# Performance work log

Measured on AMD Instinct MI355X. Metric: run time of the kernel, lower is better.

Reference implementation:

```python
import jax, jax.numpy as jnp
import numpy as np

N, P1, P2, D = 4, 8192, 8192, 3
BIG = 1e10  # masks out padded target points before top-k (pytorch3d uses +inf)


def setup_inputs() -> dict:
    key = jax.random.key(0)
    k1, k2, k3 = jax.random.split(key, 3)
    pred_points = jax.random.normal(k1, (N, P1, D), dtype=jnp.float32)
    target_points = jax.random.normal(k2, (N, P2, D), dtype=jnp.float32)
    # ragged target lengths in [P2//2, P2] (always > 0 so every batch element is 'visible')
    target_lengths = jax.random.randint(k3, (N,), P2 // 2, P2 + 1, dtype=jnp.int32)
    return {
        "pred_points": pred_points,
        "target_points": target_points,
        "target_lengths": target_lengths,
        "num_neighbours": 1,
    }


def reference(pred_points, target_points, target_lengths, num_neighbours):
    x, y = pred_points, target_points  # [N,P1,D], [N,P2,D]
    n, p1, _ = x.shape
    p2 = y.shape[1]
    x2 = jnp.sum(x * x, axis=-1)
    y2 = jnp.sum(y * y, axis=-1)
    d2 = x2[:, :, None] + y2[:, None, :] - 2.0 * jnp.einsum('nid,njd->nij', x, y)
    d2 = jnp.maximum(d2, 0.0)

    # mask of invalid (padded) target points per batch: j >= target_lengths[b]
    y_pad = jnp.arange(p2)[None, :] >= target_lengths[:, None]  # [N,P2]

    # knn_points(x -> y): invalid y columns pushed to BIG before top-k smallest
    dxy = jnp.where(y_pad[:, None, :], BIG, d2)
    nn_x = -jax.lax.top_k(-dxy, num_neighbours)[0]          # [N,P1,K]
    cham_x = jnp.sum(jnp.mean(nn_x, axis=-1), axis=1) / p1  # point_reduction='mean'

    # knn_points(y -> x): all x points valid; zero out padded y rows afterwards
    dyx = jnp.swapaxes(d2, 1, 2)                            # [N,P2,P1]
    nn_y = -jax.lax.top_k(-dyx, num_neighbours)[0]          # [N,P2,K]
    cham_y_pts = jnp.where(y_pad, 0.0, jnp.mean(nn_y, axis=-1))
    cham_y = jnp.sum(cham_y_pts, axis=1) / target_lengths.astype(x.dtype)

    # batch_reduction='mean'
    loss = (jnp.sum(cham_x) + jnp.sum(cham_y)) / n
    return loss
```

## Files before the change

kernel.cpp:

```cpp
#include <hip/hip_runtime.h>

constexpr int N = 4;
constexpr int P = 8192;
constexpr int NSEG = 8;
constexpr int SEGC = P / NSEG;
constexpr int TILE = 256;
constexpr int MI = 8;
constexpr int ROWS = 256;
constexpr int RG = P / ROWS;
constexpr size_t TRANS_F = (size_t)2 * N * P * 4;

__global__ __launch_bounds__(256) void chamfer_prep_kernel(
    const float* __restrict__ pred, const float* __restrict__ targ,
    const int* __restrict__ lens, float4* __restrict__ trans)
{
    const int i = blockIdx.x * 256 + threadIdx.x;
    const int side = i >> 15;
    const int b    = (i >> 13) & (N - 1);
    const int j    = i & (P - 1);
    const float* s = (side ? targ : pred) + ((size_t)b * P + j) * 3;
    const float x = s[0], y = s[1], z = s[2];
    float w = fmaf(x, x, fmaf(y, y, z * z));
    if (side == 1 && j >= lens[b]) w = 1e30f;
    trans[i] = make_float4(-2.f * x, -2.f * y, -2.f * z, w);
}

__global__ __launch_bounds__(256) void chamfer_min_kernel(
    const int* __restrict__ lens, const float4* __restrict__ trans,
    float* __restrict__ partial)
{
    const int seg = blockIdx.y;
    int id = blockIdx.x;
    const int rg  = id & (RG - 1); id >>= 5;
    const int b   = id & (N - 1);  id >>= 2;
    const int dir = id;
    const int row0 = rg * ROWS;
    const int c0   = seg * SEGC;
    const int L    = lens[b];
    const int tid  = threadIdx.x;
    const int chunk   = tid >> 5;
    const int rowtile = tid & 31;
    const int wave = tid >> 6, lane = tid & 63;

    float* slot = partial + (((size_t)dir * N + b) * NSEG + seg) * P + row0;
    if (dir == 1 && row0 >= L) return;
    if (dir == 0 && c0 >= L) { slot[tid] = 1e30f; return; }

    const float4* rsrc = trans + ((size_t)(dir == 0 ? 0 : 1) * N + b) * P;
    const float4* csrc = trans + ((size_t)(dir == 0 ? 1 : 0) * N + b) * P;

    float rx[MI], ry[MI], rz[MI], rw[MI], best[MI];
    #pragma unroll
    for (int k = 0; k < MI; ++k) {
        const float4 t = rsrc[row0 + rowtile + 32 * k];
        rx[k] = -0.5f * t.x; ry[k] = -0.5f * t.y; rz[k] = -0.5f * t.z;
        rw[k] = t.w;
        best[k] = 1e30f;
    }

    __shared__ float4 buf[2][TILE];
    __shared__ float  red[ROWS * 9];

    int vc = SEGC;
    if (dir == 0 && L - c0 < SEGC) vc = L - c0;
    const int nt = (vc + TILE - 1) / TILE;

    __builtin_amdgcn_global_load_lds(
        (const __attribute__((address_space(1))) void*)(csrc + c0 + wave * 64 + lane),
        (__attribute__((address_space(3))) void*)&buf[0][wave * 64], 16, 0, 0);
    __syncthreads();

    for (int t = 0; t < nt; ++t) {
        const int cur = t & 1;
        if (t + 1 < nt)
            __builtin_amdgcn_global_load_lds(
                (const __attribute__((address_space(1))) void*)(csrc + c0 + (t + 1) * TILE + wave * 64 + lane),
                (__attribute__((address_space(3))) void*)&buf[cur ^ 1][wave * 64], 16, 0, 0);

        const float4* sp = &buf[cur][chunk * 32];
        #pragma unroll 4
        for (int jj = 0; jj < 32; jj += 2) {
            const float4 q0 = sp[jj];
            const float4 q1 = sp[jj + 1];
            #pragma unroll
            for (int k = 0; k < MI; ++k) {
                float d0 = fmaf(rx[k], q0.x, fmaf(ry[k], q0.y, fmaf(rz[k], q0.z, q0.w)));
                float d1 = fmaf(rx[k], q1.x, fmaf(ry[k], q1.y, fmaf(rz[k], q1.z, q1.w)));
                best[k] = fminf(best[k], fminf(d0, d1));
            }
        }
        __syncthreads();
    }

    #pragma unroll
    for (int k = 0; k < MI; ++k)
        red[(rowtile + 32 * k) * 9 + chunk] = best[k];
    if (chunk == 0) {
        #pragma unroll
        for (int k = 0; k < MI; ++k)
            red[(rowtile + 32 * k) * 9 + 8] = rw[k];
    }
    __syncthreads();

    {
        const float* r = &red[tid * 9];
        float v = fminf(fminf(fminf(r[0], r[1]), fminf(r[2], r[3])),
                        fminf(fminf(r[4], r[5]), fminf(r[6], r[7])));
        slot[tid] = v + r[8];
    }
}

__global__ __launch_bounds__(256) void chamfer_reduce_kernel(
    const float* __restrict__ partial, const int* __restrict__ lens,
    float* __restrict__ out)
{
    const int item = blockIdx.x * 256 + threadIdx.x;
    const int dir = item >> 15;
    const int b   = (item >> 13) & (N - 1);
    const int p   = item & (P - 1);
    const int L   = lens[b];

    float c = 0.f;
    if (dir == 0 || p < L) {
        const float* base = partial + (((size_t)dir * N + b) * NSEG) * P + p;
        float v = base[0];
        #pragma unroll
        for (int s = 1; s < NSEG; ++s) v = fminf(v, base[(size_t)s * P]);
        v = fmaxf(v, 0.f);
        c = dir ? v / ((float)L * (float)N) : v * (1.0f / ((float)P * (float)N));
    }
    #pragma unroll
    for (int off = 32; off; off >>= 1) c += __shfl_down(c, off, 64);
    __shared__ float acc[4];
    if ((threadIdx.x & 63) == 0) acc[threadIdx.x >> 6] = c;
    __syncthreads();
    if (threadIdx.x == 0) atomicAdd(out, acc[0] + acc[1] + acc[2] + acc[3]);
}

extern "C" void kernel_launch(void* const* d_in, const int* in_sizes, int n_in,
                              void* d_out, int out_size, void* d_ws, size_t ws_size,
                              hipStream_t stream)
{
    const float* pred = (const float*)d_in[0];
    const float* targ = (const float*)d_in[1];
    const int*   lens = (const int*)d_in[2];
    float* out = (float*)d_out;
    float4* trans   = (float4*)d_ws;
    float*  partial = (float*)d_ws + TRANS_F;

    hipMemsetAsync(out, 0, out_size * sizeof(float), stream);
    chamfer_prep_kernel<<<(2 * N * P) / 256, 256, 0, stream>>>(pred, targ, lens, trans);
    dim3 grid(2 * N * RG, NSEG);
    chamfer_min_kernel<<<grid, 256, 0, stream>>>(lens, trans, partial);
    chamfer_reduce_kernel<<<(2 * N * P) / 256, 256, 0, stream>>>(partial, lens, out);
}
```

Baseline: 105.5 us.

## Drop LDS staging; give each thread 4 rows and read column points directly

The min kernel no longer stages column points through double-buffered LDS with global_load_lds and no longer does the cross-chunk LDS reduction. Each thread now owns 4 full rows and scans all 1024 columns of its segment, reading them straight from global memory (the same address across a wavefront, so broadcast loads through cache). Row coordinates are read from the raw inputs and the norm is recomputed in-kernel. The grid becomes 1D with 4x more rows per block, which cuts the block count and removes syncs. The trade-off is lower parallelism per block (fewer blocks) and the loss of early termination on padded columns, since the full SEGC is always scanned.

Result: slower. 132.5 us (+25.6%).

```diff
diff --git a/kernel.cpp b/kernel.cpp
--- a/kernel.cpp
+++ b/kernel.cpp
@@ -4,9 +4,8 @@
 constexpr int P = 8192;
 constexpr int NSEG = 8;
 constexpr int SEGC = P / NSEG;
-constexpr int TILE = 256;
-constexpr int MI = 8;
-constexpr int ROWS = 256;
+constexpr int MI = 4;
+constexpr int ROWS = 256 * MI;
 constexpr int RG = P / ROWS;
 constexpr size_t TRANS_F = (size_t)2 * N * P * 4;
 
@@ -26,88 +25,56 @@
 }
 
 __global__ __launch_bounds__(256) void chamfer_min_kernel(
+    const float* __restrict__ pred, const float* __restrict__ targ,
     const int* __restrict__ lens, const float4* __restrict__ trans,
     float* __restrict__ partial)
 {
-    const int seg = blockIdx.y;
-    int id = blockIdx.x;
-    const int rg  = id & (RG - 1); id >>= 5;
-    const int b   = id & (N - 1);  id >>= 2;
-    const int dir = id;
+    const int x   = blockIdx.x;
+    const int dir = x >> 8;
+    const int b   = (x >> 6) & (N - 1);
+    const int rg  = (x >> 3) & (RG - 1);
+    const int seg = x & (NSEG - 1);
     const int row0 = rg * ROWS;
     const int c0   = seg * SEGC;
     const int L    = lens[b];
     const int tid  = threadIdx.x;
-    const int chunk   = tid >> 5;
-    const int rowtile = tid & 31;
-    const int wave = tid >> 6, lane = tid & 63;
 
     float* slot = partial + (((size_t)dir * N + b) * NSEG + seg) * P + row0;
+
     if (dir == 1 && row0 >= L) return;
-    if (dir == 0 && c0 >= L) { slot[tid] = 1e30f; return; }
+    if (dir == 0 && c0 >= L) {
+        #pragma unroll
+        for (int k = 0; k < MI; ++k) slot[tid + 256 * k] = 1e30f;
+        return;
+    }
 
-    const float4* rsrc = trans + ((size_t)(dir == 0 ? 0 : 1) * N + b) * P;
-    const float4* csrc = trans + ((size_t)(dir == 0 ? 1 : 0) * N + b) * P;
+    const float* rbase = (dir == 0 ? pred : targ) + (size_t)b * P * 3;
+    const float4* __restrict__ csrc =
+        trans + ((size_t)(dir == 0 ? 1 : 0) * N + b) * P + c0;
 
-    float rx[MI], ry[MI], rz[MI], rw[MI], best[MI];
+    float rx[MI], ry[MI], rz[MI], x2[MI], best[MI];
     #pragma unroll
     for (int k = 0; k < MI; ++k) {
-        const float4 t = rsrc[row0 + rowtile + 32 * k];
-        rx[k] = -0.5f * t.x; ry[k] = -0.5f * t.y; rz[k] = -0.5f * t.z;
-        rw[k] = t.w;
+        const float* p = rbase + (size_t)(row0 + tid + 256 * k) * 3;
+        rx[k] = p[0]; ry[k] = p[1]; rz[k] = p[2];
+        x2[k] = fmaf(rx[k], rx[k], fmaf(ry[k], ry[k], rz[k] * rz[k]));
         best[k] = 1e30f;
     }
 
-    __shared__ float4 buf[2][TILE];
-    __shared__ float  red[ROWS * 9];
-
-    int vc = SEGC;
-    if (dir == 0 && L - c0 < SEGC) vc = L - c0;
-    const int nt = (vc + TILE - 1) / TILE;
-
-    __builtin_amdgcn_global_load_lds(
-        (const __attribute__((address_space(1))) void*)(csrc + c0 + wave * 64 + lane),
-        (__attribute__((address_space(3))) void*)&buf[0][wave * 64], 16, 0, 0);
-    __syncthreads();
-
-    for (int t = 0; t < nt; ++t) {
-        const int cur = t & 1;
-        if (t + 1 < nt)
-            __builtin_amdgcn_global_load_lds(
-                (const __attribute__((address_space(1))) void*)(csrc + c0 + (t + 1) * TILE + wave * 64 + lane),
-                (__attribute__((address_space(3))) void*)&buf[cur ^ 1][wave * 64], 16, 0, 0);
-
-        const float4* sp = &buf[cur][chunk * 32];
-        #pragma unroll 4
-        for (int jj = 0; jj < 32; jj += 2) {
-            const float4 q0 = sp[jj];
-            const float4 q1 = sp[jj + 1];
-            #pragma unroll
-            for (int k = 0; k < MI; ++k) {
-                float d0 = fmaf(rx[k], q0.x, fmaf(ry[k], q0.y, fmaf(rz[k], q0.z, q0.w)));
-                float d1 = fmaf(rx[k], q1.x, fmaf(ry[k], q1.y, fmaf(rz[k], q1.z, q1.w)));
-                best[k] = fminf(best[k], fminf(d0, d1));
-            }
+    #pragma unroll 4
+    for (int j = 0; j < SEGC; j += 2) {
+        const float4 q0 = csrc[j];
+        const float4 q1 = csrc[j + 1];
+        #pragma unroll
+        for (int k = 0; k < MI; ++k) {
+            float d0 = fmaf(rx[k], q0.x, fmaf(ry[k], q0.y, fmaf(rz[k], q0.z, q0.w)));
+            float d1 = fmaf(rx[k], q1.x, fmaf(ry[k], q1.y, fmaf(rz[k], q1.z, q1.w)));
+            best[k] = fminf(best[k], fminf(d0, d1));
         }
-        __syncthreads();
     }
 
     #pragma unroll
-    for (int k = 0; k < MI; ++k)
-        red[(rowtile + 32 * k) * 9 + chunk] = best[k];
-    if (chunk == 0) {
-        #pragma unroll
-        for (int k = 0; k < MI; ++k)
-            red[(rowtile + 32 * k) * 9 + 8] = rw[k];
-    }
-    __syncthreads();
-
-    {
-        const float* r = &red[tid * 9];
-        float v = fminf(fminf(fminf(r[0], r[1]), fminf(r[2], r[3])),
-                        fminf(fminf(r[4], r[5]), fminf(r[6], r[7])));
-        slot[tid] = v + r[8];
-    }
+    for (int k = 0; k < MI; ++k) slot[tid + 256 * k] = best[k] + x2[k];
 }
 
 __global__ __launch_bounds__(256) void chamfer_reduce_kernel(
@@ -150,7 +117,6 @@
 
     hipMemsetAsync(out, 0, out_size * sizeof(float), stream);
     chamfer_prep_kernel<<<(2 * N * P) / 256, 256, 0, stream>>>(pred, targ, lens, trans);
-    dim3 grid(2 * N * RG, NSEG);
-    chamfer_min_kernel<<<grid, 256, 0, stream>>>(lens, trans, partial);
+    chamfer_min_kernel<<<2 * N * RG * NSEG, 256, 0, stream>>>(pred, targ, lens, trans, partial);
     chamfer_reduce_kernel<<<(2 * N * P) / 256, 256, 0, stream>>>(partial, lens, out);
 }
```
